# Performance work log

Measured on AMD Instinct MI355X. Metric: run time of the kernel, lower is better.

## Reference

```python
import jax, jax.numpy as jnp
import numpy as np

B, D, T_STEPS = 256, 512, 256


def setup_inputs() -> dict:
    key = jax.random.key(0)
    k1, k2 = jax.random.split(key)
    # Scale K like flax lecun_normal init (std = 1/sqrt(fan_in)) so rollout stays stable.
    z0 = jax.random.normal(k1, (B, D), dtype=jnp.float32)
    K = jax.random.normal(k2, (D, D), dtype=jnp.float32) / np.sqrt(D)
    return {"z0": z0, "K": K, "T": T_STEPS}


def reference(z0, K, T):
    # z_{t+1} = z_t @ K  (flax Linear with use_bias=False: y = x @ kernel)
    def step(z, _):
        z_next = z @ K  # [B, D] @ [D, D] -> [B, D]
        return z_next, z_next

    _, preds = jax.lax.scan(step, z0, xs=None, length=T)  # [T, B, D]
    return jnp.transpose(preds, (1, 0, 2))  # [B, T, D]
```

## Files before the change

kernel.cpp:

```cpp
#include <hip/hip_runtime.h>


typedef unsigned short u16;
typedef unsigned int u32;
typedef __bf16 bf16x8 __attribute__((ext_vector_type(8)));
typedef float f32x4 __attribute__((ext_vector_type(4)));
typedef u16 u16x4 __attribute__((ext_vector_type(4)));
typedef u16 u16x8 __attribute__((ext_vector_type(8)));

#define MAT 262144
#define SLOT 1048576
#define WSLOT 131072

__device__ __forceinline__ u16 f2b(float f) {
  u32 x = __float_as_uint(f);
  return (u16)((x + 0x7fffu + ((x >> 16) & 1u)) >> 16);
}
__device__ __forceinline__ float b2f(u16 u) { return __uint_as_float(((u32)u) << 16); }

__device__ __forceinline__ size_t pidx(int r, int k) {
  return (size_t)(((r >> 4) * 16 + (k >> 5)) * 512 + ((k >> 3) & 3) * 128 + (r & 15) * 8 + (k & 7));
}

__device__ __forceinline__ void gll16(const void* g, void* l) {
  __builtin_amdgcn_global_load_lds((__attribute__((address_space(1))) void*)(void*)g,
                                   (__attribute__((address_space(3))) void*)l, 16, 0, 0);
}

__global__ __launch_bounds__(256) void prep_kernel(const float* __restrict__ Kc,
                                                   const float* __restrict__ z0,
                                                   u16* __restrict__ P,
                                                   u16* __restrict__ W0,
                                                   u16* __restrict__ z0lo) {
  int tid = threadIdx.x, b = blockIdx.x;
  if (b < 64) {
    int r0 = (b >> 3) * 64, c0b = (b & 7) * 64;
#pragma unroll
    for (int q = 0; q < 2; ++q) {
      int g = q * 256 + tid;
      int r = r0 + (g >> 3), c0 = c0b + (g & 7) * 8;
      float4 v0 = *(const float4*)(Kc + (size_t)r * 512 + c0);
      float4 v1 = *(const float4*)(Kc + (size_t)r * 512 + c0 + 4);
      float v[8] = {v0.x, v0.y, v0.z, v0.w, v1.x, v1.y, v1.z, v1.w};
      u16x8 h8, l8v;
#pragma unroll
      for (int j = 0; j < 8; ++j) {
        u16 h = f2b(v[j]);
        h8[j] = h;
        l8v[j] = f2b(v[j] - b2f(h));
        size_t ib = pidx(c0 + j, r);
        P[2 * MAT + ib] = h;
        P[3 * MAT + ib] = l8v[j];
      }
      size_t ia = pidx(r, c0);
      *(u16x8*)(P + ia) = h8;
      *(u16x8*)(P + MAT + ia) = l8v;
    }
  } else {
    int idb = b - 64;
#pragma unroll
    for (int q = 0; q < 4; ++q) {
      int g = (idb * 4 + q) * 256 + tid;
      int r = g >> 6, c0 = (g & 63) * 8;
      float4 v0 = *(const float4*)(z0 + (size_t)r * 512 + c0);
      float4 v1 = *(const float4*)(z0 + (size_t)r * 512 + c0 + 4);
      float v[8] = {v0.x, v0.y, v0.z, v0.w, v1.x, v1.y, v1.z, v1.w};
      u16x8 h8, l8v;
#pragma unroll
      for (int j = 0; j < 8; ++j) {
        u16 h = f2b(v[j]);
        h8[j] = h;
        l8v[j] = f2b(v[j] - b2f(h));
      }
      size_t ia = pidx(r, c0);
      *(u16x8*)(W0 + ia) = h8;
      *(u16x8*)(z0lo + ia) = l8v;
    }
  }
}

__global__ __launch_bounds__(256, 2) void gemm_split(
    const u16* __restrict__ A0h, const u16* __restrict__ A0l, long Astr,
    const u16* __restrict__ B0h, long Bstr,
    u16* __restrict__ C0, long Cstr, int wmode) {
  __shared__ u16 Bs[32768];
  int z = blockIdx.z;
  const u16* Ah = A0h + (size_t)z * Astr;
  const u16* Al = A0l + (size_t)z * Astr;
  const u16* Bh = B0h + (size_t)z * Bstr;
  const u16* Bl = Bh + MAT;
  u16* C = C0 + (size_t)z * Cstr;
  int tid = threadIdx.x;
  int m0 = blockIdx.y * 64, n0 = blockIdx.x * 32;
  int wv = tid >> 6, lane = tid & 63;
  int mrow = lane & 15, quad = lane >> 4;
  int l8 = lane * 8;
  int nchunk0 = n0 >> 4;
  const u16* ph = Bh + (size_t)nchunk0 * 16 * 512;
  const u16* pl = Bl + (size_t)nchunk0 * 16 * 512;
#pragma unroll
  for (int i = 0; i < 8; ++i) {
    int ch = wv * 8 + i;
    gll16(ph + (size_t)ch * 512 + l8, Bs + ch * 512);
    gll16(pl + (size_t)ch * 512 + l8, Bs + 16384 + ch * 512);
  }
  __syncthreads();
  int mc = (m0 >> 4) + wv;
  f32x4 acc[2] = {};
#pragma unroll 4
  for (int kt = 0; kt < 16; ++kt) {
    size_t co = (size_t)(mc * 16 + kt) * 512 + l8;
    bf16x8 ah = *(const bf16x8*)(Ah + co);
    bf16x8 al = *(const bf16x8*)(Al + co);
#pragma unroll
    for (int nt = 0; nt < 2; ++nt) {
      bf16x8 bh = *(const bf16x8*)(Bs + (nt * 16 + kt) * 512 + l8);
      bf16x8 bl = *(const bf16x8*)(Bs + 16384 + (nt * 16 + kt) * 512 + l8);
      acc[nt] = __builtin_amdgcn_mfma_f32_16x16x32_bf16(ah, bh, acc[nt], 0, 0, 0);
      acc[nt] = __builtin_amdgcn_mfma_f32_16x16x32_bf16(al, bh, acc[nt], 0, 0, 0);
      acc[nt] = __builtin_amdgcn_mfma_f32_16x16x32_bf16(ah, bl, acc[nt], 0, 0, 0);
    }
  }
  int mbase = m0 + wv * 16 + quad * 4;
#pragma unroll
  for (int nt = 0; nt < 2; ++nt) {
    int n = n0 + nt * 16 + mrow;
    if (wmode == 0) {
      u16x4 h4, l4;
#pragma unroll
      for (int r = 0; r < 4; ++r) {
        float v = acc[nt][r];
        u16 h = f2b(v), l = f2b(v - b2f(h));
        size_t ia = pidx(mbase + r, n);
        C[ia] = h;
        C[MAT + ia] = l;
        h4[r] = h;
        l4[r] = l;
      }
      size_t ib = pidx(n, mbase);
      *(u16x4*)(C + 2 * MAT + ib) = h4;
      *(u16x4*)(C + 3 * MAT + ib) = l4;
    } else {
#pragma unroll
      for (int r = 0; r < 4; ++r) C[pidx(mbase + r, n)] = f2b(acc[nt][r]);
    }
  }
}

__global__ __launch_bounds__(256, 2) void gemm_out(const u16* __restrict__ Wb,
                                                   const u16* __restrict__ PT0,
                                                   float* __restrict__ out) {
  __shared__ u16 Bs[32768];
  int z = blockIdx.z;
  const u16* A = Wb + (size_t)(z >> 4) * WSLOT;
  const u16* Bt = PT0 + (size_t)(z & 15) * SLOT;
  int tid = threadIdx.x;
  int n0 = blockIdx.x * 64;
  int wv = tid >> 6, lane = tid & 63;
  int mrow = lane & 15, quad = lane >> 4;
  int l8 = lane * 8;
  const u16* pb = Bt + (size_t)(n0 >> 4) * 16 * 512;
#pragma unroll
  for (int i = 0; i < 16; ++i) {
    int ch = wv * 16 + i;
    gll16(pb + (size_t)ch * 512 + l8, Bs + ch * 512);
  }
  __syncthreads();
  int mc0 = wv * 4;
  f32x4 acc[4][4] = {};
#pragma unroll 4
  for (int kt = 0; kt < 16; ++kt) {
    bf16x8 a[4], b[4];
#pragma unroll
    for (int mt = 0; mt < 4; ++mt)
      a[mt] = *(const bf16x8*)(A + (size_t)((mc0 + mt) * 16 + kt) * 512 + l8);
#pragma unroll
    for (int nt = 0; nt < 4; ++nt)
      b[nt] = *(const bf16x8*)(Bs + (nt * 16 + kt) * 512 + l8);
#pragma unroll
    for (int mt = 0; mt < 4; ++mt)
#pragma unroll
      for (int nt = 0; nt < 4; ++nt)
        acc[mt][nt] = __builtin_amdgcn_mfma_f32_16x16x32_bf16(a[mt], b[nt], acc[mt][nt], 0, 0, 0);
  }
#pragma unroll
  for (int mt = 0; mt < 4; ++mt)
#pragma unroll
    for (int nt = 0; nt < 4; ++nt) {
      int gb = wv * 64 + mt * 16 + quad * 4;
      int gd = n0 + nt * 16 + mrow;
#pragma unroll
      for (int r = 0; r < 4; ++r)
        out[((size_t)(gb + r) * 256 + z) * 512 + gd] = acc[mt][nt][r];
    }
}

extern "C" void kernel_launch(void* const* d_in, const int* in_sizes, int n_in,
                              void* d_out, int out_size, void* d_ws, size_t ws_size,
                              hipStream_t stream) {
  const float* z0 = (const float*)d_in[0];
  const float* Kc = (const float*)d_in[1];
  float* out = (float*)d_out;
  u16* W = (u16*)d_ws;
  u16* z0l = W + 16 * WSLOT;
  u16* P = z0l + WSLOT;
  auto S = [&](int s) { return P + (size_t)s * SLOT; };
  dim3 blk(256);

  prep_kernel<<<80, blk, 0, stream>>>(Kc, z0, P, W, z0l);
  gemm_split<<<dim3(16, 8, 1), blk, 0, stream>>>(S(0), S(0) + MAT, 0, S(0) + 2 * MAT, 0, S(1), 0, 0);
  gemm_split<<<dim3(16, 8, 2), blk, 0, stream>>>(S(0), S(0) + MAT, SLOT, S(1) + 2 * MAT, 0, S(2), SLOT, 0);
  gemm_split<<<dim3(16, 8, 4), blk, 0, stream>>>(S(0), S(0) + MAT, SLOT, S(3) + 2 * MAT, 0, S(4), SLOT, 0);
  gemm_split<<<dim3(16, 8, 8), blk, 0, stream>>>(S(0), S(0) + MAT, SLOT, S(7) + 2 * MAT, 0, S(8), SLOT, 0);
  gemm_split<<<dim3(16, 8, 1), blk, 0, stream>>>(S(15), S(15) + MAT, 0, S(15) + 2 * MAT, 0, S(16), 0, 0);
  gemm_split<<<dim3(16, 8, 2), blk, 0, stream>>>(S(16), S(16) + MAT, 0, S(15) + 2 * MAT, SLOT, S(17), SLOT, 0);
  gemm_split<<<dim3(16, 8, 4), blk, 0, stream>>>(S(18), S(18) + MAT, 0, S(15) + 2 * MAT, SLOT, S(19), SLOT, 0);
  gemm_split<<<dim3(16, 8, 7), blk, 0, stream>>>(S(22), S(22) + MAT, 0, S(15) + 2 * MAT, SLOT, S(23), SLOT, 0);
  gemm_split<<<dim3(16, 4, 15), blk, 0, stream>>>(W, z0l, 0, S(15) + 2 * MAT, SLOT, W + WSLOT, WSLOT, 1);
  gemm_out<<<dim3(8, 1, 256), blk, 0, stream>>>(W, P + 2 * MAT, out);
}
```

Measured before the change: 260.7 us.

## Replace power-table stages with doubling rollout fused into matrix-squaring launches

The old schedule builds all K^1..K^16 and K^16..K^256 power tables, then applies 15 powers to z0 in a separate launch. The new schedule squares K repeatedly (K^16, K^32, K^64, K^128) and, in the same launches, extends the z-state table by doubling (z·K^16, z·K^32 and so on). It also skips writing row-major or transposed low parts that later stages never read, using per-slice masks. This removes a launch and much redundant GEMM work and global writes. In exchange it adds branchy per-block role selection and a longer serial chain of dependent squarings, which may change error accumulation in the split-bf16 precision scheme.

```diff
diff --git a/kernel.cpp b/kernel.cpp
--- a/kernel.cpp
+++ b/kernel.cpp
@@ -30,8 +30,8 @@
 __global__ __launch_bounds__(256) void prep_kernel(const float* __restrict__ Kc,
                                                    const float* __restrict__ z0,
                                                    u16* __restrict__ P,
-                                                   u16* __restrict__ W0,
-                                                   u16* __restrict__ z0lo) {
+                                                   u16* __restrict__ Uh,
+                                                   u16* __restrict__ Ul) {
   int tid = threadIdx.x, b = blockIdx.x;
   if (b < 64) {
     int r0 = (b >> 3) * 64, c0b = (b & 7) * 64;
@@ -73,25 +73,49 @@
         l8v[j] = f2b(v[j] - b2f(h));
       }
       size_t ia = pidx(r, c0);
-      *(u16x8*)(W0 + ia) = h8;
-      *(u16x8*)(z0lo + ia) = l8v;
-    }
-  }
-}
-
-__global__ __launch_bounds__(256, 2) void gemm_split(
-    const u16* __restrict__ A0h, const u16* __restrict__ A0l, long Astr,
-    const u16* __restrict__ B0h, long Bstr,
-    u16* __restrict__ C0, long Cstr, int wmode) {
+      *(u16x8*)(Uh + ia) = h8;
+      *(u16x8*)(Ul + ia) = l8v;
+    }
+  }
+}
+
+__global__ __launch_bounds__(256, 2) void gemm_stage(
+    const u16* __restrict__ fA, long fAstr,
+    u16* __restrict__ fC, long fCstr,
+    const u16* __restrict__ Bh, int nfull, int rowmask, int tlomask,
+    const u16* __restrict__ UA, u16* __restrict__ UC) {
   __shared__ u16 Bs[32768];
-  int z = blockIdx.z;
-  const u16* Ah = A0h + (size_t)z * Astr;
-  const u16* Al = A0l + (size_t)z * Astr;
-  const u16* Bh = B0h + (size_t)z * Bstr;
+  int z = blockIdx.z, y = blockIdx.y;
+  const u16 *Ah, *Al;
+  u16 *Ch, *Clo, *CTh, *CTl;
+  int m0;
+  bool full = (y < 8 * nfull);
+  bool wrow, wtlo;
+  if (full) {
+    Ah = fA + (size_t)z * fAstr;
+    Al = Ah + MAT;
+    Ch = fC + (size_t)z * fCstr;
+    Clo = Ch + MAT;
+    CTh = Ch + 2 * MAT;
+    CTl = Ch + 3 * MAT;
+    m0 = y * 64;
+    wrow = (rowmask >> z) & 1;
+    wtlo = (tlomask >> z) & 1;
+  } else {
+    int yy = y - 8 * nfull;
+    int u = yy >> 2;
+    Ah = UA + (size_t)u * WSLOT;
+    Al = Ah + 16 * (size_t)WSLOT;
+    Ch = UC + (size_t)u * WSLOT;
+    Clo = Ch + 16 * (size_t)WSLOT;
+    CTh = CTl = nullptr;
+    m0 = (yy & 3) * 64;
+    wrow = true;
+    wtlo = false;
+  }
   const u16* Bl = Bh + MAT;
-  u16* C = C0 + (size_t)z * Cstr;
   int tid = threadIdx.x;
-  int m0 = blockIdx.y * 64, n0 = blockIdx.x * 32;
+  int n0 = blockIdx.x * 32;
   int wv = tid >> 6, lane = tid & 63;
   int mrow = lane & 15, quad = lane >> 4;
   int l8 = lane * 8;
@@ -125,24 +149,26 @@
 #pragma unroll
   for (int nt = 0; nt < 2; ++nt) {
     int n = n0 + nt * 16 + mrow;
-    if (wmode == 0) {
-      u16x4 h4, l4;
+    u16x4 h4, l4;
+#pragma unroll
+    for (int r = 0; r < 4; ++r) {
+      float v = acc[nt][r];
+      u16 h = f2b(v);
+      h4[r] = h;
+      l4[r] = f2b(v - b2f(h));
+    }
+    if (wrow) {
 #pragma unroll
       for (int r = 0; r < 4; ++r) {
-        float v = acc[nt][r];
-        u16 h = f2b(v), l = f2b(v - b2f(h));
         size_t ia = pidx(mbase + r, n);
-        C[ia] = h;
-        C[MAT + ia] = l;
-        h4[r] = h;
-        l4[r] = l;
+        Ch[ia] = h4[r];
+        Clo[ia] = l4[r];
       }
+    }
+    if (full) {
       size_t ib = pidx(n, mbase);
-      *(u16x4*)(C + 2 * MAT + ib) = h4;
-      *(u16x4*)(C + 3 * MAT + ib) = l4;
-    } else {
-#pragma unroll
-      for (int r = 0; r < 4; ++r) C[pidx(mbase + r, n)] = f2b(acc[nt][r]);
+      *(u16x4*)(CTh + ib) = h4;
+      if (wtlo) *(u16x4*)(CTl + ib) = l4;
     }
   }
 }
@@ -201,21 +227,20 @@
   const float* z0 = (const float*)d_in[0];
   const float* Kc = (const float*)d_in[1];
   float* out = (float*)d_out;
-  u16* W = (u16*)d_ws;
-  u16* z0l = W + 16 * WSLOT;
-  u16* P = z0l + WSLOT;
+  u16* Uh = (u16*)d_ws;
+  u16* Ul = Uh + 16 * (size_t)WSLOT;
+  u16* P = Ul + 16 * (size_t)WSLOT;
   auto S = [&](int s) { return P + (size_t)s * SLOT; };
   dim3 blk(256);
 
-  prep_kernel<<<80, blk, 0, stream>>>(Kc, z0, P, W, z0l);
-  gemm_split<<<dim3(16, 8, 1), blk, 0, stream>>>(S(0), S(0) + MAT, 0, S(0) + 2 * MAT, 0, S(1), 0, 0);
-  gemm_split<<<dim3(16, 8, 2), blk, 0, stream>>>(S(0), S(0) + MAT, SLOT, S(1) + 2 * MAT, 0, S(2), SLOT, 0);
-  gemm_split<<<dim3(16, 8, 4), blk, 0, stream>>>(S(0), S(0) + MAT, SLOT, S(3) + 2 * MAT, 0, S(4), SLOT, 0);
-  gemm_split<<<dim3(16, 8, 8), blk, 0, stream>>>(S(0), S(0) + MAT, SLOT, S(7) + 2 * MAT, 0, S(8), SLOT, 0);
-  gemm_split<<<dim3(16, 8, 1), blk, 0, stream>>>(S(15), S(15) + MAT, 0, S(15) + 2 * MAT, 0, S(16), 0, 0);
-  gemm_split<<<dim3(16, 8, 2), blk, 0, stream>>>(S(16), S(16) + MAT, 0, S(15) + 2 * MAT, SLOT, S(17), SLOT, 0);
-  gemm_split<<<dim3(16, 8, 4), blk, 0, stream>>>(S(18), S(18) + MAT, 0, S(15) + 2 * MAT, SLOT, S(19), SLOT, 0);
-  gemm_split<<<dim3(16, 8, 7), blk, 0, stream>>>(S(22), S(22) + MAT, 0, S(15) + 2 * MAT, SLOT, S(23), SLOT, 0);
-  gemm_split<<<dim3(16, 4, 15), blk, 0, stream>>>(W, z0l, 0, S(15) + 2 * MAT, SLOT, W + WSLOT, WSLOT, 1);
-  gemm_out<<<dim3(8, 1, 256), blk, 0, stream>>>(W, P + 2 * MAT, out);
-}
+  prep_kernel<<<80, blk, 0, stream>>>(Kc, z0, P, Uh, Ul);
+  gemm_stage<<<dim3(16, 8, 1), blk, 0, stream>>>(S(0), 0, S(1), 0, S(0) + 2 * MAT, 1, 0x1, 0x1, nullptr, nullptr);
+  gemm_stage<<<dim3(16, 8, 2), blk, 0, stream>>>(S(0), SLOT, S(2), SLOT, S(1) + 2 * MAT, 1, 0x3, 0x2, nullptr, nullptr);
+  gemm_stage<<<dim3(16, 8, 4), blk, 0, stream>>>(S(0), SLOT, S(4), SLOT, S(3) + 2 * MAT, 1, 0xF, 0x8, nullptr, nullptr);
+  gemm_stage<<<dim3(16, 8, 8), blk, 0, stream>>>(S(0), SLOT, S(8), SLOT, S(7) + 2 * MAT, 1, 0x80, 0x80, nullptr, nullptr);
+  gemm_stage<<<dim3(16, 12, 1), blk, 0, stream>>>(S(15), 0, S(16), 0, S(15) + 2 * MAT, 1, 0x1, 0x1, Uh, Uh + 1 * (size_t)WSLOT);
+  gemm_stage<<<dim3(16, 16, 1), blk, 0, stream>>>(S(16), 0, S(17), 0, S(16) + 2 * MAT, 1, 0x1, 0x1, Uh, Uh + 2 * (size_t)WSLOT);
+  gemm_stage<<<dim3(16, 24, 1), blk, 0, stream>>>(S(17), 0, S(18), 0, S(17) + 2 * MAT, 1, 0x0, 0x1, Uh, Uh + 4 * (size_t)WSLOT);
+  gemm_stage<<<dim3(16, 32, 1), blk, 0, stream>>>(S(18), 0, S(18), 0, S(18) + 2 * MAT, 0, 0x0, 0x0, Uh, Uh + 8 * (size_t)WSLOT);
+  gemm_out<<<dim3(8, 1, 256), blk, 0, stream>>>(Uh, P + 2 * MAT, out);
+}
```

Result: faster. 248.9 us (-4.5%).
